# Kernel optimization log

Measured on AMD Instinct MI355X. Metric: run time of the kernel, lower is better.

The kernel has to match this reference:

```python
import math
import jax, jax.numpy as jnp
import numpy as np

B, T, C = 4, 2048, 1024
NH, HD = 16, 64  # n_head, head_dim
RANK = 128


def setup_inputs() -> dict:
    key = jax.random.key(0)
    ks = jax.random.split(key, 9)
    s_in = 1.0 / math.sqrt(C)
    s_r = 1.0 / math.sqrt(RANK)
    inp = {"x": jax.random.normal(ks[0], (B, T, C), dtype=jnp.float32)}
    for i, name in enumerate(["q", "k", "v", "c"]):
        inp[name + "A"] = jax.random.normal(ks[1 + 2 * i], (RANK, C), dtype=jnp.float32) * s_in
        inp[name + "B"] = jax.random.normal(ks[2 + 2 * i], (C, RANK), dtype=jnp.float32) * s_r
    return inp


def _lowrank(x, A, Bf):
    # HarmonicLinear: rank-r factorized linear, W = Bf @ A, y = x @ W^T
    return (x @ A.T) @ Bf.T


def reference(x, qA, qB, kA, kB, vA, vB, cA, cB):
    b, t, c = x.shape
    q = _lowrank(x, qA, qB).reshape(b, t, NH, HD).transpose(0, 2, 1, 3)  # [b,h,t,d]
    k = _lowrank(x, kA, kB).reshape(b, t, NH, HD).transpose(0, 2, 1, 3)
    v = _lowrank(x, vA, vB).reshape(b, t, NH, HD).transpose(0, 2, 1, 3)
    att = jnp.einsum("bhqd,bhkd->bhqk", q, k) * (1.0 / math.sqrt(HD))
    causal = jnp.tril(jnp.ones((t, t), dtype=bool))
    att = jnp.where(causal, att, -jnp.inf)
    att = jax.nn.softmax(att, axis=-1)
    y = jnp.einsum("bhqk,bhkd->bhqd", att, v)
    y = y.transpose(0, 2, 1, 3).reshape(b, t, c)
    return _lowrank(y, cA, cB)
```

## Files before the change

### kernel.cpp

```cpp
#include <hip/hip_runtime.h>

typedef unsigned short u16;
typedef __attribute__((ext_vector_type(8))) short bf16x8;
typedef __attribute__((ext_vector_type(4))) float f32x4;
typedef __attribute__((ext_vector_type(16))) float f32x16;
typedef __attribute__((ext_vector_type(4))) int i32x4;

typedef const __attribute__((address_space(1))) void gvoid_t;
typedef __attribute__((address_space(3))) void svoid_t;

__device__ __forceinline__ u16 f2bf(float f) {
  unsigned u = __builtin_bit_cast(unsigned, f);
  u += 0x7fffu + ((u >> 16) & 1u);
  return (u16)(u >> 16);
}

__device__ __forceinline__ unsigned cvtpk(float a, float b) {
  unsigned r;
  asm("v_cvt_pk_bf16_f32 %0, %1, %2" : "=v"(r) : "v"(a), "v"(b));
  return r;
}

__device__ __forceinline__ void gload_lds16(const u16* g, u16* ldsbase) {
  __builtin_amdgcn_global_load_lds((gvoid_t*)g, (svoid_t*)ldsbase, 16, 0, 0);
}

__device__ __forceinline__ void mfma16(f32x4& d, bf16x8 a, bf16x8 b) {
  asm("v_mfma_f32_16x16x32_bf16 %0, %1, %2, %0" : "+v"(d) : "v"(a), "v"(b));
}
__device__ __forceinline__ void mfma32(f32x16& d, bf16x8 a, bf16x8 b) {
  asm("v_mfma_f32_32x32x16_bf16 %0, %1, %2, %0" : "+v"(d) : "v"(a), "v"(b));
}
__device__ __forceinline__ void mfma_fence4(f32x4& a, f32x4& b, f32x4& c, f32x4& d) {
  asm volatile("s_nop 7\n\ts_nop 7" : "+v"(a), "+v"(b), "+v"(c), "+v"(d));
}
__device__ __forceinline__ void fence16x2(f32x16& a, f32x16& b) {
  asm volatile("s_nop 7\n\ts_nop 7\n\ts_nop 7" : "+v"(a), "+v"(b));
}

__global__ __launch_bounds__(256) void cvt_x_kernel(const float* __restrict__ src,
                                                    u16* __restrict__ dst) {
  int i = (blockIdx.x * 256 + threadIdx.x) * 4;
  float4 v = *(const float4*)(src + i);
  ushort4 o = {f2bf(v.x), f2bf(v.y), f2bf(v.z), f2bf(v.w)};
  *(ushort4*)(dst + i) = o;
}

struct W8 { const float* s[8]; };
__global__ __launch_bounds__(256) void cvt_w_kernel(W8 w, u16* __restrict__ dst) {
  const float* src = w.s[blockIdx.y];
  u16* d = dst + (size_t)blockIdx.y * 131072;
  int i = (blockIdx.x * 256 + threadIdx.x) * 4;
  float4 v = *(const float4*)(src + i);
  ushort4 o = {f2bf(v.x), f2bf(v.y), f2bf(v.z), f2bf(v.w)};
  *(ushort4*)(d + i) = o;
}

struct G3 { const u16* A[3]; const u16* B[3]; void* C[3]; float osc[3]; };

template <typename OutT, bool VT_OUT, int BM>
__global__ __launch_bounds__(256) void gemm_nt(G3 g, int M, int N, int K) {
  constexpr int NI = (BM == 128) ? 4 : 2;
  __shared__ __align__(16) u16 At[2][BM * 64];
  __shared__ __align__(16) u16 Bt[2][128 * 64];
  const int z = blockIdx.z;
  const u16* __restrict__ A = g.A[z];
  const u16* __restrict__ Bw = g.B[z];
  const float osc = g.osc[z];
  const int tid = threadIdx.x;
  const int lane = tid & 63, w = tid >> 6;
  const int wm = (BM == 128) ? (w >> 1) : 0;
  const int wn = (BM == 128) ? (w & 1) : w;
  constexpr int WNW = (BM == 128) ? 64 : 32;
  const int l15 = lane & 15, l4 = lane >> 4;
  const int row0 = blockIdx.x * BM, col0 = blockIdx.y * 128;
  const int srow = lane >> 3;
  const int schunk = ((lane & 7) ^ srow) * 8;
  const u16* Ag = A + (size_t)(row0 + w * 8 + srow) * K + schunk;
  const u16* Bg = Bw + (size_t)(col0 + w * 8 + srow) * K + schunk;
  f32x4 acc[4][NI] = {};
  auto STAGE = [&](int k0, int buf) {
#pragma unroll
    for (int i = 0; i < BM / 32; ++i)
      gload_lds16(Ag + (size_t)i * 32 * K + k0, &At[buf][(w * 8 + i * 32) * 64]);
#pragma unroll
    for (int i = 0; i < 4; ++i)
      gload_lds16(Bg + (size_t)i * 32 * K + k0, &Bt[buf][(w * 8 + i * 32) * 64]);
  };
  STAGE(0, 0);
  asm volatile("s_waitcnt vmcnt(0)" ::: "memory");
  __syncthreads();
  const int nk = K >> 6;
  for (int t = 0; t < nk; ++t) {
    const int cur = t & 1;
    if (t + 1 < nk) STAGE((t + 1) << 6, cur ^ 1);
#pragma unroll
    for (int kk = 0; kk < 64; kk += 32) {
      bf16x8 af[4], bfr[NI];
#pragma unroll
      for (int mi = 0; mi < 4; ++mi) {
        const int r = wm * 64 + mi * 16 + l15;
        af[mi] = *(const bf16x8*)&At[cur][r * 64 + ((kk + 8 * l4) ^ ((r & 7) << 3))];
      }
#pragma unroll
      for (int ni = 0; ni < NI; ++ni) {
        const int r = wn * WNW + ni * 16 + l15;
        bfr[ni] = *(const bf16x8*)&Bt[cur][r * 64 + ((kk + 8 * l4) ^ ((r & 7) << 3))];
      }
#pragma unroll
      for (int mi = 0; mi < 4; ++mi)
#pragma unroll
        for (int ni = 0; ni < NI; ++ni) mfma16(acc[mi][ni], af[mi], bfr[ni]);
    }
    asm volatile("s_waitcnt vmcnt(0)" ::: "memory");
    __syncthreads();
  }
#pragma unroll
  for (int mi = 0; mi < 4; ++mi)
    mfma_fence4(acc[mi][0], acc[mi][NI - 1], acc[mi][0], acc[mi][NI - 1]);
  if constexpr (VT_OUT) {
    u16* VTo = (u16*)g.C[z];
    const int bbv = row0 >> 11;
#pragma unroll
    for (int mi = 0; mi < 4; ++mi) {
      const int r = row0 + wm * 64 + mi * 16 + l4 * 4;
      const int t0 = r & 2047;
#pragma unroll
      for (int ni = 0; ni < NI; ++ni) {
        const int c = col0 + wn * WNW + ni * 16 + l15;
        ushort4 ov = {f2bf(acc[mi][ni][0] * osc), f2bf(acc[mi][ni][1] * osc),
                      f2bf(acc[mi][ni][2] * osc), f2bf(acc[mi][ni][3] * osc)};
        *(ushort4*)(VTo + ((size_t)(bbv * 1024 + c)) * 2048 + t0) = ov;
      }
    }
  } else {
    OutT* __restrict__ C = (OutT*)g.C[z];
#pragma unroll
    for (int mi = 0; mi < 4; ++mi) {
      const int r = row0 + wm * 64 + mi * 16 + l4 * 4;
#pragma unroll
      for (int ni = 0; ni < NI; ++ni) {
        const int c = col0 + wn * WNW + ni * 16 + l15;
#pragma unroll
        for (int j = 0; j < 4; ++j) {
          float v = acc[mi][ni][j] * osc;
          if constexpr (sizeof(OutT) == 2)
            ((u16*)C)[(size_t)(r + j) * N + c] = f2bf(v);
          else
            ((float*)C)[(size_t)(r + j) * N + c] = v;
        }
      }
    }
  }
}

__global__ __launch_bounds__(256, 4) void attn_kernel(const u16* __restrict__ Qg,
                                                      const u16* __restrict__ Kg,
                                                      const u16* __restrict__ VTg,
                                                      u16* __restrict__ Yg) {
  __shared__ __align__(16) u16 Kt[2][64 * 64];
  __shared__ __align__(16) u16 Vt[2][64 * 64];
  const int tid = threadIdx.x;
  const int lane = tid & 63, w = tid >> 6;
  const int l31 = lane & 31, hi = lane >> 5;
  const int f = blockIdx.x;
  const int gq = f >> 6;
  int qt;
  if (gq < 4) qt = gq;
  else if (gq < 8) qt = 19 - gq;
  else if (gq < 12) qt = gq - 4;
  else qt = 23 - gq;
  const int bhid = f & 63;
  const int bb = bhid >> 4, h = bhid & 15;
  const size_t rb = (size_t)bb * 2048;
  const int h64 = h * 64;
  const int qb0 = qt << 7;
  const int qg = qb0 + w * 32 + l31;
  const int qend = qb0 + w * 32 + 31;
  const u16* Kbh = Kg + rb * 1024 + h64;
  const u16* VTbh = VTg + (size_t)bhid * 64 * 2048;
  const int srow = lane >> 3;
  const int schunk = ((lane & 7) ^ srow) * 8;

  bf16x8 qf[4];
#pragma unroll
  for (int kd = 0; kd < 4; ++kd)
    qf[kd] = *(const bf16x8*)(Qg + (rb + qg) * 1024 + h64 + kd * 16 + 8 * hi);

  f32x16 o0 = {}, o1 = {};
  const float MNEG = -30000.f;
  float lrun = 0.f;

  auto STAGE = [&](int it, int buf) {
    const int kv0 = it << 6;
    const int r0 = w * 16;
#pragma unroll
    for (int i = 0; i < 2; ++i) {
      gload_lds16(Kbh + (size_t)(kv0 + r0 + i * 8 + srow) * 1024 + schunk,
                  &Kt[buf][(r0 + i * 8) * 64]);
      gload_lds16(VTbh + (size_t)(r0 + i * 8 + srow) * 2048 + kv0 + schunk,
                  &Vt[buf][(r0 + i * 8) * 64]);
    }
  };
  STAGE(0, 0);
  asm volatile("s_waitcnt vmcnt(0)" ::: "memory");
  __syncthreads();

  const int nkv = 2 * qt + 2;
  for (int t = 0; t < nkv; ++t) {
    const int cur = t & 1;
    if (t + 1 < nkv) STAGE(t + 1, cur ^ 1);
    const int kv0 = t << 6;
    if (kv0 <= qend) {
      f32x16 s0 = {}, s1 = {};
      __builtin_amdgcn_s_setprio(1);
#pragma unroll
      for (int kd = 0; kd < 4; ++kd) {
        const int col = (kd * 16 + 8 * hi) ^ ((l31 & 7) << 3);
        bf16x8 kf0 = *(const bf16x8*)&Kt[cur][l31 * 64 + col];
        bf16x8 kf1 = *(const bf16x8*)&Kt[cur][(32 + l31) * 64 + col];
        mfma32(s0, kf0, qf[kd]);
        mfma32(s1, kf1, qf[kd]);
      }
      __builtin_amdgcn_s_setprio(0);
      fence16x2(s0, s1);
      if (kv0 + 63 > qb0 + w * 32) {
        const int lim = qg - (kv0 + 4 * hi);
#pragma unroll
        for (int r = 0; r < 16; ++r) {
          const int C0 = (r & 3) + 8 * (r >> 2);
          if (C0 > lim) s0[r] = MNEG;
          if (C0 + 32 > lim) s1[r] = MNEG;
        }
      }
#pragma unroll
      for (int r = 0; r < 16; ++r) {
        s0[r] = exp2f(s0[r]);
        s1[r] = exp2f(s1[r]);
      }
      float t8[8];
#pragma unroll
      for (int r = 0; r < 8; ++r)
        t8[r] = (s0[2 * r] + s0[2 * r + 1]) + (s1[2 * r] + s1[2 * r + 1]);
      float rs = ((t8[0] + t8[1]) + (t8[2] + t8[3])) +
                 ((t8[4] + t8[5]) + (t8[6] + t8[7]));
      lrun += rs + __shfl_xor(rs, 32, 64);
      i32x4 paw[4];
#pragma unroll
      for (int tl = 0; tl < 2; ++tl) {
        const f32x16& p = tl ? s1 : s0;
#pragma unroll
        for (int ks = 0; ks < 2; ++ks) {
          unsigned pk0 = cvtpk(p[8 * ks + 0], p[8 * ks + 1]);
          unsigned pk1 = cvtpk(p[8 * ks + 2], p[8 * ks + 3]);
          unsigned pk2 = cvtpk(p[8 * ks + 4], p[8 * ks + 5]);
          unsigned pk3 = cvtpk(p[8 * ks + 6], p[8 * ks + 7]);
          unsigned x0 = (unsigned)__shfl_xor((int)pk0, 32, 64);
          unsigned x1 = (unsigned)__shfl_xor((int)pk1, 32, 64);
          unsigned x2 = (unsigned)__shfl_xor((int)pk2, 32, 64);
          unsigned x3 = (unsigned)__shfl_xor((int)pk3, 32, 64);
          i32x4 A;
          A[0] = (int)(hi ? x2 : pk0);
          A[1] = (int)(hi ? x3 : pk1);
          A[2] = (int)(hi ? pk2 : x0);
          A[3] = (int)(hi ? pk3 : x1);
          paw[tl * 2 + ks] = A;
        }
      }
      asm volatile("s_nop 1");
      __builtin_amdgcn_s_setprio(1);
#pragma unroll
      for (int tl = 0; tl < 2; ++tl)
#pragma unroll
        for (int ks = 0; ks < 2; ++ks) {
          bf16x8 pa = __builtin_bit_cast(bf16x8, paw[tl * 2 + ks]);
          const int kvc = tl * 32 + ks * 16 + 8 * hi;
#pragma unroll
          for (int dt = 0; dt < 2; ++dt) {
            const int row = dt * 32 + l31;
            bf16x8 vf = *(const bf16x8*)&Vt[cur][row * 64 + (kvc ^ ((l31 & 7) << 3))];
            if (dt == 0) mfma32(o0, vf, pa);
            else         mfma32(o1, vf, pa);
          }
        }
      __builtin_amdgcn_s_setprio(0);
    }
    asm volatile("s_waitcnt vmcnt(0)" ::: "memory");
    __syncthreads();
  }
  fence16x2(o0, o1);
  const float inv = 1.f / lrun;
  u16* Yrow = Yg + (rb + qg) * 1024 + h64;
#pragma unroll
  for (int r = 0; r < 16; r += 2) {
    const int dbase = (r & 3) + 8 * (r >> 2) + 4 * hi;
    *(unsigned*)(Yrow + dbase) = cvtpk(o0[r] * inv, o0[r + 1] * inv);
    *(unsigned*)(Yrow + 32 + dbase) = cvtpk(o1[r] * inv, o1[r + 1] * inv);
  }
}

extern "C" void kernel_launch(void* const* d_in, const int* in_sizes, int n_in,
                              void* d_out, int out_size, void* d_ws, size_t ws_size,
                              hipStream_t stream) {
  const float* x = (const float*)d_in[0];
  char* ws = (char*)d_ws;
  u16* xb = (u16*)ws;
  u16* wb = (u16*)(ws + (16u << 20));
  u16* Rq = (u16*)(ws + (18u << 20));
  u16* Rk = (u16*)(ws + (20u << 20));
  u16* Rv = (u16*)(ws + (22u << 20));
  u16* Ry = (u16*)(ws + (24u << 20));
  u16* Qb = (u16*)(ws + (26u << 20));
  u16* Kb = (u16*)(ws + (42u << 20));
  u16* VT = (u16*)(ws + (58u << 20));
  const int WSZ = 131072;
  const float SC = 0.18033688011112042f;

  cvt_x_kernel<<<8192, 256, 0, stream>>>(x, xb);
  W8 wp;
  for (int i = 0; i < 8; ++i) wp.s[i] = (const float*)d_in[1 + i];
  cvt_w_kernel<<<dim3(128, 8), 256, 0, stream>>>(wp, wb);

  G3 g1;
  g1.A[0] = g1.A[1] = g1.A[2] = xb;
  g1.B[0] = wb; g1.B[1] = wb + 2 * WSZ; g1.B[2] = wb + 4 * WSZ;
  g1.C[0] = Rq; g1.C[1] = Rk; g1.C[2] = Rv;
  g1.osc[0] = g1.osc[1] = g1.osc[2] = 1.f;
  gemm_nt<u16, false, 64><<<dim3(128, 1, 3), 256, 0, stream>>>(g1, 8192, 128, 1024);

  G3 g2;
  g2.A[0] = Rq; g2.A[1] = Rk; g2.A[2] = Rk;
  g2.B[0] = wb + 1 * WSZ; g2.B[1] = wb + 3 * WSZ; g2.B[2] = wb + 3 * WSZ;
  g2.C[0] = Qb; g2.C[1] = Kb; g2.C[2] = Kb;
  g2.osc[0] = SC; g2.osc[1] = 1.f; g2.osc[2] = 1.f;
  gemm_nt<u16, false, 128><<<dim3(64, 8, 2), 256, 0, stream>>>(g2, 8192, 1024, 128);
  G3 g2v;
  g2v.A[0] = g2v.A[1] = g2v.A[2] = Rv;
  g2v.B[0] = g2v.B[1] = g2v.B[2] = wb + 5 * WSZ;
  g2v.C[0] = g2v.C[1] = g2v.C[2] = VT;
  g2v.osc[0] = g2v.osc[1] = g2v.osc[2] = 1.f;
  gemm_nt<u16, true, 128><<<dim3(64, 8, 1), 256, 0, stream>>>(g2v, 8192, 1024, 128);

  attn_kernel<<<dim3(1024), 256, 0, stream>>>(Qb, Kb, VT, xb);

  G3 g3;
  g3.A[0] = g3.A[1] = g3.A[2] = xb;
  g3.B[0] = g3.B[1] = g3.B[2] = wb + 6 * WSZ;
  g3.C[0] = g3.C[1] = g3.C[2] = Ry;
  g3.osc[0] = g3.osc[1] = g3.osc[2] = 1.f;
  gemm_nt<u16, false, 64><<<dim3(128, 1, 1), 256, 0, stream>>>(g3, 8192, 128, 1024);
  G3 g4;
  g4.A[0] = g4.A[1] = g4.A[2] = Ry;
  g4.B[0] = g4.B[1] = g4.B[2] = wb + 7 * WSZ;
  g4.C[0] = g4.C[1] = g4.C[2] = d_out;
  g4.osc[0] = g4.osc[1] = g4.osc[2] = 1.f;
  gemm_nt<float, false, 128><<<dim3(64, 8, 1), 256, 0, stream>>>(g4, 8192, 1024, 128);
}
```

Before: 149.6 us.

## Merge conversion and Q/K/V up-projection launches, schedule attention longest-first

Fuses the x and weight fp32-to-bf16 conversions into a single launch. It also merges the Q/K and V^T up-projection GEMMs into one launch, choosing the transposed-output epilogue per z-slice with a runtime flag instead of a template parameter. The attention grid's zig-zag query-tile ordering is replaced by a simple longest-causal-tile-first ordering. These changes cut launch count and tail idle time, at the cost of a runtime branch in the GEMM epilogue and a different load-balancing pattern in attention.

```diff
diff --git a/kernel.cpp b/kernel.cpp
--- a/kernel.cpp
+++ b/kernel.cpp
@@ -38,27 +38,31 @@
   asm volatile("s_nop 7\n\ts_nop 7\n\ts_nop 7" : "+v"(a), "+v"(b));
 }
 
-__global__ __launch_bounds__(256) void cvt_x_kernel(const float* __restrict__ src,
-                                                    u16* __restrict__ dst) {
-  int i = (blockIdx.x * 256 + threadIdx.x) * 4;
+struct W8 { const float* s[8]; };
+__global__ __launch_bounds__(256) void cvt_all_kernel(const float* __restrict__ x,
+                                                      W8 w, u16* __restrict__ xb,
+                                                      u16* __restrict__ wb) {
+  const int b = blockIdx.x;
+  const float* src;
+  u16* dst;
+  int i;
+  if (b < 8192) {
+    src = x; dst = xb;
+    i = (b * 256 + (int)threadIdx.x) * 4;
+  } else {
+    const int wi = (b - 8192) >> 7;
+    const int wo = (b - 8192) & 127;
+    src = w.s[wi]; dst = wb + (size_t)wi * 131072;
+    i = (wo * 256 + (int)threadIdx.x) * 4;
+  }
   float4 v = *(const float4*)(src + i);
   ushort4 o = {f2bf(v.x), f2bf(v.y), f2bf(v.z), f2bf(v.w)};
   *(ushort4*)(dst + i) = o;
 }
 
-struct W8 { const float* s[8]; };
-__global__ __launch_bounds__(256) void cvt_w_kernel(W8 w, u16* __restrict__ dst) {
-  const float* src = w.s[blockIdx.y];
-  u16* d = dst + (size_t)blockIdx.y * 131072;
-  int i = (blockIdx.x * 256 + threadIdx.x) * 4;
-  float4 v = *(const float4*)(src + i);
-  ushort4 o = {f2bf(v.x), f2bf(v.y), f2bf(v.z), f2bf(v.w)};
-  *(ushort4*)(d + i) = o;
-}
-
-struct G3 { const u16* A[3]; const u16* B[3]; void* C[3]; float osc[3]; };
-
-template <typename OutT, bool VT_OUT, int BM>
+struct G3 { const u16* A[3]; const u16* B[3]; void* C[3]; float osc[3]; int vt[3]; };
+
+template <typename OutT, int BM>
 __global__ __launch_bounds__(256) void gemm_nt(G3 g, int M, int N, int K) {
   constexpr int NI = (BM == 128) ? 4 : 2;
   __shared__ __align__(16) u16 At[2][BM * 64];
@@ -118,7 +122,7 @@
 #pragma unroll
   for (int mi = 0; mi < 4; ++mi)
     mfma_fence4(acc[mi][0], acc[mi][NI - 1], acc[mi][0], acc[mi][NI - 1]);
-  if constexpr (VT_OUT) {
+  if (g.vt[z]) {
     u16* VTo = (u16*)g.C[z];
     const int bbv = row0 >> 11;
 #pragma unroll
@@ -164,12 +168,7 @@
   const int lane = tid & 63, w = tid >> 6;
   const int l31 = lane & 31, hi = lane >> 5;
   const int f = blockIdx.x;
-  const int gq = f >> 6;
-  int qt;
-  if (gq < 4) qt = gq;
-  else if (gq < 8) qt = 19 - gq;
-  else if (gq < 12) qt = gq - 4;
-  else qt = 23 - gq;
+  const int qt = 15 - (f >> 6);
   const int bhid = f & 63;
   const int bb = bhid >> 4, h = bhid & 15;
   const size_t rb = (size_t)bb * 2048;
@@ -316,30 +315,25 @@
   const int WSZ = 131072;
   const float SC = 0.18033688011112042f;
 
-  cvt_x_kernel<<<8192, 256, 0, stream>>>(x, xb);
   W8 wp;
   for (int i = 0; i < 8; ++i) wp.s[i] = (const float*)d_in[1 + i];
-  cvt_w_kernel<<<dim3(128, 8), 256, 0, stream>>>(wp, wb);
+  cvt_all_kernel<<<8192 + 1024, 256, 0, stream>>>(x, wp, xb, wb);
 
   G3 g1;
   g1.A[0] = g1.A[1] = g1.A[2] = xb;
   g1.B[0] = wb; g1.B[1] = wb + 2 * WSZ; g1.B[2] = wb + 4 * WSZ;
   g1.C[0] = Rq; g1.C[1] = Rk; g1.C[2] = Rv;
   g1.osc[0] = g1.osc[1] = g1.osc[2] = 1.f;
-  gemm_nt<u16, false, 64><<<dim3(128, 1, 3), 256, 0, stream>>>(g1, 8192, 128, 1024);
+  g1.vt[0] = g1.vt[1] = g1.vt[2] = 0;
+  gemm_nt<u16, 64><<<dim3(128, 1, 3), 256, 0, stream>>>(g1, 8192, 128, 1024);
 
   G3 g2;
-  g2.A[0] = Rq; g2.A[1] = Rk; g2.A[2] = Rk;
-  g2.B[0] = wb + 1 * WSZ; g2.B[1] = wb + 3 * WSZ; g2.B[2] = wb + 3 * WSZ;
-  g2.C[0] = Qb; g2.C[1] = Kb; g2.C[2] = Kb;
+  g2.A[0] = Rq; g2.A[1] = Rk; g2.A[2] = Rv;
+  g2.B[0] = wb + 1 * WSZ; g2.B[1] = wb + 3 * WSZ; g2.B[2] = wb + 5 * WSZ;
+  g2.C[0] = Qb; g2.C[1] = Kb; g2.C[2] = VT;
   g2.osc[0] = SC; g2.osc[1] = 1.f; g2.osc[2] = 1.f;
-  gemm_nt<u16, false, 128><<<dim3(64, 8, 2), 256, 0, stream>>>(g2, 8192, 1024, 128);
-  G3 g2v;
-  g2v.A[0] = g2v.A[1] = g2v.A[2] = Rv;
-  g2v.B[0] = g2v.B[1] = g2v.B[2] = wb + 5 * WSZ;
-  g2v.C[0] = g2v.C[1] = g2v.C[2] = VT;
-  g2v.osc[0] = g2v.osc[1] = g2v.osc[2] = 1.f;
-  gemm_nt<u16, true, 128><<<dim3(64, 8, 1), 256, 0, stream>>>(g2v, 8192, 1024, 128);
+  g2.vt[0] = 0; g2.vt[1] = 0; g2.vt[2] = 1;
+  gemm_nt<u16, 128><<<dim3(64, 8, 3), 256, 0, stream>>>(g2, 8192, 1024, 128);
 
   attn_kernel<<<dim3(1024), 256, 0, stream>>>(Qb, Kb, VT, xb);
 
@@ -348,11 +342,13 @@
   g3.B[0] = g3.B[1] = g3.B[2] = wb + 6 * WSZ;
   g3.C[0] = g3.C[1] = g3.C[2] = Ry;
   g3.osc[0] = g3.osc[1] = g3.osc[2] = 1.f;
-  gemm_nt<u16, false, 64><<<dim3(128, 1, 1), 256, 0, stream>>>(g3, 8192, 128, 1024);
+  g3.vt[0] = g3.vt[1] = g3.vt[2] = 0;
+  gemm_nt<u16, 64><<<dim3(128, 1, 1), 256, 0, stream>>>(g3, 8192, 128, 1024);
   G3 g4;
   g4.A[0] = g4.A[1] = g4.A[2] = Ry;
   g4.B[0] = g4.B[1] = g4.B[2] = wb + 7 * WSZ;
   g4.C[0] = g4.C[1] = g4.C[2] = d_out;
   g4.osc[0] = g4.osc[1] = g4.osc[2] = 1.f;
-  gemm_nt<float, false, 128><<<dim3(64, 8, 1), 256, 0, stream>>>(g4, 8192, 1024, 128);
-}
+  g4.vt[0] = g4.vt[1] = g4.vt[2] = 0;
+  gemm_nt<float, 128><<<dim3(64, 8, 1), 256, 0, stream>>>(g4, 8192, 1024, 128);
+}
```

New measurement: 144.3 us. -3.6%, faster.
